# Optimization experiments

Hardware: AMD Instinct MI355X
Metric: run time of the kernel (lower is better)

The kernel has to match this reference:

```python
import jax, jax.numpy as jnp
import numpy as np

EPS = 1e-3  # kernel epsilon used in Performer generalized kernel
B, H, N, D, M = 1, 8, 1024, 64, 128  # batch, heads, seq, dim_heads, nb_features


def _gaussian_orthogonal_matrix(m, d, seed=0):
    # GaussianOrthogonalRandomMatrix with scaling=0: stacked QR blocks, rows
    # rescaled by chi-distributed norms of gaussian d-vectors.
    rng = np.random.default_rng(seed)
    blocks = []
    for _ in range(m // d):
        g = rng.standard_normal((d, d))
        qmat, _ = np.linalg.qr(g)
        blocks.append(qmat.T)
    proj = np.concatenate(blocks, axis=0)  # [m, d], orthonormal rows per block
    mult = np.linalg.norm(rng.standard_normal((m, d)), axis=1)  # chi norms
    return (mult[:, None] * proj).astype(np.float32)


def setup_inputs() -> dict:
    key = jax.random.key(0)
    kq, kk, kv = jax.random.split(key, 3)
    q = jax.random.normal(kq, (B, H, N, D), dtype=jnp.float32)
    k = jax.random.normal(kk, (B, H, N, D), dtype=jnp.float32)
    v = jax.random.normal(kv, (B, H, N, D), dtype=jnp.float32)
    proj = jnp.asarray(_gaussian_orthogonal_matrix(M, D))
    return {"q": q, "k": k, "v": v, "proj": proj}


def _generalized_kernel(x, proj):
    # kernel_fn(relu)( (x / d**0.25) @ proj^T ) + eps
    normalizer = 1.0 / (x.shape[-1] ** 0.25)
    xp = jnp.einsum('bhnd,md->bhnm', x * normalizer, proj)
    return jax.nn.relu(xp) + EPS


def reference(q, k, v, proj):
    qp = _generalized_kernel(q, proj)  # [B,H,N,M]
    kp = _generalized_kernel(k, proj)  # [B,H,N,M]
    # causal linear attention
    k_cumsum = jnp.cumsum(kp, axis=-2)                              # [B,H,N,M]
    context = jnp.einsum('bhnm,bhne->bhnme', kp, v)                 # [B,H,N,M,D]
    context = jnp.cumsum(context, axis=-3)                          # prefix sums over n
    context = context / k_cumsum[..., None]                         # normalize
    out = jnp.einsum('bhnme,bhnm->bhne', context, qp)               # [B,H,N,D]
    return out
```

## Files before the change

kernel.cpp:

```cpp
#include <hip/hip_runtime.h>

static constexpr int H = 8, N = 1024, D = 64, M = 128;
static constexpr float EPS = 1e-3f;
static constexpr float NORM = 0.35355339059327373f;

typedef __attribute__((ext_vector_type(8))) short short8;
typedef __attribute__((ext_vector_type(4))) float f32x4;

__device__ inline unsigned short f2bf(float x) {
    unsigned u = __float_as_uint(x);
    return (unsigned short)((u + 0x7fffu + ((u >> 16) & 1u)) >> 16);
}
__device__ inline float bf2f(unsigned short u) {
    return __uint_as_float(((unsigned)u) << 16);
}
__device__ inline ushort4 pack4(float4 g) {
    return (ushort4){f2bf(g.x), f2bf(g.y), f2bf(g.z), f2bf(g.w)};
}

__global__ __launch_bounds__(512) void k_projg(const float* __restrict__ q,
                                               const float* __restrict__ k,
                                               const float* __restrict__ proj,
                                               const float* __restrict__ v,
                                               unsigned short* __restrict__ qpb,
                                               unsigned short* __restrict__ kpb,
                                               unsigned short* __restrict__ Gpb,
                                               float* __restrict__ kpart) {
    __shared__ __align__(16) short smem[30208];
    short* projb = smem;
    short* xb = smem + 9216;
    short* obuf = smem + 13824;
    short* kpT = smem + 22528;
    short* vT = smem + 27648;
    const int tid = threadIdx.x;
    const int rblk = blockIdx.x;
    const int h = blockIdx.y;
    const int rowbase = h * N + rblk * 32;
    const int lane = tid & 63, wv = tid >> 6;
    const int rt = wv & 3, mh = wv >> 2;
    const int fr = lane & 15, fq = lane >> 4;

    {
        int r = tid >> 4, dq = tid & 15;
        float4 g = *(const float4*)&q[(rowbase + r) * D + dq * 4];
        float4 gk = *(const float4*)&k[(rowbase + r) * D + dq * 4];
        int rv = tid & 31, e4 = (tid >> 5) * 4;
        float4 gv = *(const float4*)&v[(rowbase + rv) * D + e4];
        g.x *= NORM; g.y *= NORM; g.z *= NORM; g.w *= NORM;
        *(ushort4*)&xb[r * 72 + dq * 4] = pack4(g);
        gk.x *= NORM; gk.y *= NORM; gk.z *= NORM; gk.w *= NORM;
        *(ushort4*)&xb[(32 + r) * 72 + dq * 4] = pack4(gk);
        vT[(e4 + 0) * 40 + rv] = (short)f2bf(gv.x);
        vT[(e4 + 1) * 40 + rv] = (short)f2bf(gv.y);
        vT[(e4 + 2) * 40 + rv] = (short)f2bf(gv.z);
        vT[(e4 + 3) * 40 + rv] = (short)f2bf(gv.w);
    }
    for (int i4 = tid; i4 < 2048; i4 += 512) {
        int m = i4 >> 4, dq = i4 & 15;
        *(ushort4*)&projb[m * 72 + dq * 4] = pack4(*(const float4*)&proj[i4 * 4]);
    }
    __syncthreads();

    f32x4 accp[4];
#pragma unroll
    for (int i = 0; i < 4; i++) accp[i] = (f32x4){0.f, 0.f, 0.f, 0.f};
#pragma unroll
    for (int kt = 0; kt < 2; kt++) {
        short8 a = *(const short8*)&xb[(16 * rt + fr) * 72 + kt * 32 + fq * 8];
#pragma unroll
        for (int i = 0; i < 4; i++) {
            const int mt = mh * 4 + i;
            short8 bb = *(const short8*)&projb[(16 * mt + fr) * 72 + kt * 32 + fq * 8];
            accp[i] = __builtin_amdgcn_mfma_f32_16x16x32_bf16(a, bb, accp[i], 0, 0, 0);
        }
    }
#pragma unroll
    for (int i = 0; i < 4; i++) {
        const int mt = mh * 4 + i;
#pragma unroll
        for (int reg = 0; reg < 4; reg++) {
            const int r = 16 * rt + fq * 4 + reg;
            const int m = 16 * mt + fr;
            unsigned short bv = f2bf(fmaxf(accp[i][reg], 0.f) + EPS);
            obuf[r * 136 + m] = (short)bv;
            if (rt >= 2) kpT[m * 40 + (r - 32)] = (short)bv;
        }
    }
    __syncthreads();

    for (int i = tid; i < 1024; i += 512) {
        int r = i >> 4, cu8 = i & 15;
        short8 val = *(const short8*)&obuf[r * 136 + cu8 * 8];
        unsigned short* g = (r < 32) ? &qpb[(rowbase + r) * M + cu8 * 8]
                                     : &kpb[(rowbase + r - 32) * M + cu8 * 8];
        *(short8*)g = val;
    }
    const int gb = h * 32 + rblk;
    {
        const int m = tid >> 2, qr = tid & 3;
        float part = 0.f;
#pragma unroll
        for (int r = 0; r < 8; r++)
            part += bf2f((unsigned short)kpT[m * 40 + qr * 8 + r]);
        float t2;
        t2 = __shfl_xor(part, 1, 4); part += t2;
        t2 = __shfl_xor(part, 2, 4); part += t2;
        if (qr == 0) kpart[gb * M + m] = part;
    }
    __syncthreads();

    f32x4 gacc[4];
#pragma unroll
    for (int et = 0; et < 4; et++) gacc[et] = (f32x4){0.f, 0.f, 0.f, 0.f};
    {
        short8 a = *(const short8*)&kpT[(16 * wv + fr) * 40 + fq * 8];
#pragma unroll
        for (int et = 0; et < 4; et++) {
            short8 bb = *(const short8*)&vT[(16 * et + fr) * 40 + fq * 8];
            gacc[et] = __builtin_amdgcn_mfma_f32_16x16x32_bf16(a, bb, gacc[et], 0, 0, 0);
        }
    }
#pragma unroll
    for (int et = 0; et < 4; et++)
#pragma unroll
        for (int reg = 0; reg < 4; reg++) {
            const int m = 16 * wv + fq * 4 + reg;
            obuf[m * 68 + 16 * et + fr] = (short)f2bf(gacc[et][reg]);
        }
    __syncthreads();
    for (int i = tid; i < 2048; i += 512) {
        int m = i >> 4, e4 = (i & 15) * 4;
        *(ushort4*)&Gpb[(gb * M + m) * D + e4] = *(const ushort4*)&obuf[m * 68 + e4];
    }
}

__global__ __launch_bounds__(512) void k_prefix(const float* __restrict__ kpart,
                                                const unsigned short* __restrict__ Gpb,
                                                float* __restrict__ zpre,
                                                unsigned short* __restrict__ S0pre) {
    const int tid = threadIdx.x;
    const int qr = tid & 3, s0 = qr * 8;
    const int eg = (blockIdx.x << 7) | (tid >> 2);
    const int h = eg >> 13, eb = eg & 8191;

    float g[8];
#pragma unroll
    for (int r = 0; r < 8; r++)
        g[r] = bf2f(Gpb[(h * 32 + s0 + r) * (M * D) + eb]);
    float part = 0.f;
#pragma unroll
    for (int r = 0; r < 8; r++) part += g[r];
    float incl = part, tt;
    tt = __shfl_up(incl, 1, 4); if (qr >= 1) incl += tt;
    tt = __shfl_up(incl, 2, 4); if (qr >= 2) incl += tt;
    tt = __shfl_up(incl, 1, 4);
    float a = (qr == 0) ? 0.f : tt;
    unsigned short o[8];
#pragma unroll
    for (int r = 0; r < 8; r++) {
        o[r] = f2bf(a);
        a += g[r];
    }
#pragma unroll
    for (int r = 0; r < 8; r++)
        S0pre[(h * 32 + s0 + r) * (M * D) + eb] = o[r];

    if (blockIdx.x < 8) {
        const int hh = blockIdx.x;
        const int m = tid >> 2;
        float kv[8];
#pragma unroll
        for (int r = 0; r < 8; r++) kv[r] = kpart[(hh * 32 + s0 + r) * M + m];
        float p2 = 0.f;
#pragma unroll
        for (int r = 0; r < 8; r++) p2 += kv[r];
        float i2 = p2, t2;
        t2 = __shfl_up(i2, 1, 4); if (qr >= 1) i2 += t2;
        t2 = __shfl_up(i2, 2, 4); if (qr >= 2) i2 += t2;
        t2 = __shfl_up(i2, 1, 4);
        float z = (qr == 0) ? 0.f : t2;
#pragma unroll
        for (int r = 0; r < 8; r++) {
            zpre[(hh * 32 + s0 + r) * M + m] = z;
            z += kv[r];
        }
    }
}

__global__ __launch_bounds__(512) void k_attn(const unsigned short* __restrict__ qpb,
                                              const unsigned short* __restrict__ kpb,
                                              const float* __restrict__ zpre,
                                              const unsigned short* __restrict__ S0pre,
                                              const float* __restrict__ v,
                                              float* __restrict__ out) {
    __shared__ __align__(16) short smem[25600];
    short* bufW = smem;
    short* bufK = smem + 4352;
    short* bufQ = smem + 8704;
    short* s0t  = smem + 13056;
    short* vT   = smem + 21760;
    short* bufP = smem + 24320;
    const int tid = threadIdx.x;
    const int b = blockIdx.x;
    const int h = b >> 5, s = b & 31;
    const int rowstart = h * N + s * 32;
    const int lane = tid & 63, wv = tid >> 6;
    const int rt = wv & 1, js = wv >> 1;
    const int fr = lane & 15, fq = lane >> 4;

    const int sj = tid >> 4, smu = tid & 15;
    short8 kpre = *(const short8*)&kpb[(rowstart + sj) * M + smu * 8];
    short8 qpre = *(const short8*)&qpb[(rowstart + sj) * M + smu * 8];
    const int pm = tid >> 2, peb = (tid & 3) * 16;
    const unsigned short* s0src = &S0pre[(h * 32 + s) * (M * D) + pm * D + peb];
    short8 s0a = *(const short8*)&s0src[0];
    short8 s0b = *(const short8*)&s0src[8];
    const int ve4 = (tid & 15) * 4;
    float4 gv = *(const float4*)&v[(rowstart + sj) * D + ve4];
    const float zinit = zpre[(h * 32 + s) * M + pm];

    *(short8*)&bufK[sj * 136 + smu * 8] = kpre;
    *(short8*)&bufQ[sj * 136 + smu * 8] = qpre;
#pragma unroll
    for (int j = 0; j < 8; j++) {
        s0t[(peb + j) * 136 + pm] = s0a[j];
        s0t[(peb + 8 + j) * 136 + pm] = s0b[j];
    }
    vT[(ve4 + 0) * 40 + sj] = (short)f2bf(gv.x);
    vT[(ve4 + 1) * 40 + sj] = (short)f2bf(gv.y);
    vT[(ve4 + 2) * 40 + sj] = (short)f2bf(gv.z);
    vT[(ve4 + 3) * 40 + sj] = (short)f2bf(gv.w);
    __syncthreads();

    {
        const int zm = tid >> 2, qr = tid & 3, r0 = qr * 8;
        float kv[8];
        float part = 0.f;
#pragma unroll
        for (int r = 0; r < 8; r++) {
            kv[r] = bf2f((unsigned short)bufK[(r0 + r) * 136 + zm]);
            part += kv[r];
        }
        float incl = part, t;
        t = __shfl_up(incl, 1, 4); if (qr >= 1) incl += t;
        t = __shfl_up(incl, 2, 4); if (qr >= 2) incl += t;
        t = __shfl_up(incl, 1, 4);
        float z = zinit + ((qr == 0) ? 0.f : t);
#pragma unroll
        for (int r = 0; r < 8; r++) {
            const int rr = r0 + r;
            z += kv[r];
            bufW[rr * 136 + zm] = (short)f2bf(
                bf2f((unsigned short)bufQ[rr * 136 + zm]) *
                __builtin_amdgcn_rcpf(z));
        }
    }
    __syncthreads();

    f32x4 acc2 = (f32x4){0.f, 0.f, 0.f, 0.f};
#pragma unroll
    for (int kt = 0; kt < 4; kt++) {
        short8 a = *(const short8*)&bufW[(16 * rt + fr) * 136 + kt * 32 + fq * 8];
        short8 bb = *(const short8*)&s0t[(16 * js + fr) * 136 + kt * 32 + fq * 8];
        acc2 = __builtin_amdgcn_mfma_f32_16x16x32_bf16(a, bb, acc2, 0, 0, 0);
    }
    if (wv < 4) {
        const int jt = wv >> 1;
        f32x4 acc1 = (f32x4){0.f, 0.f, 0.f, 0.f};
#pragma unroll
        for (int kt = 0; kt < 4; kt++) {
            short8 a = *(const short8*)&bufW[(16 * rt + fr) * 136 + kt * 32 + fq * 8];
            short8 bb = *(const short8*)&bufK[(16 * jt + fr) * 136 + kt * 32 + fq * 8];
            acc1 = __builtin_amdgcn_mfma_f32_16x16x32_bf16(a, bb, acc1, 0, 0, 0);
        }
        const int j = 16 * jt + fr;
#pragma unroll
        for (int reg = 0; reg < 4; reg++) {
            const int nloc = 16 * rt + fq * 4 + reg;
            float val = (j <= nloc) ? acc1[reg] : 0.f;
            bufP[nloc * 40 + j] = (short)f2bf(val);
        }
    }
    __syncthreads();

    {
        short8 a = *(const short8*)&bufP[(16 * rt + fr) * 40 + fq * 8];
        short8 bb = *(const short8*)&vT[(16 * js + fr) * 40 + fq * 8];
        acc2 = __builtin_amdgcn_mfma_f32_16x16x32_bf16(a, bb, acc2, 0, 0, 0);
    }

#pragma unroll
    for (int reg = 0; reg < 4; reg++) {
        out[(rowstart + 16 * rt + fq * 4 + reg) * D + 16 * js + fr] = acc2[reg];
    }
}

extern "C" void kernel_launch(void* const* d_in, const int* in_sizes, int n_in,
                              void* d_out, int out_size, void* d_ws, size_t ws_size,
                              hipStream_t stream) {
    const float* q = (const float*)d_in[0];
    const float* k = (const float*)d_in[1];
    const float* v = (const float*)d_in[2];
    const float* proj = (const float*)d_in[3];
    float* out = (float*)d_out;

    float* ws = (float*)d_ws;
    float* kpart = ws;
    unsigned short* qpb = (unsigned short*)(kpart + H * 32 * M);
    unsigned short* kpb = qpb + H * N * M;
    unsigned short* Gpb = kpb + H * N * M;
    float* zpre = (float*)(Gpb + H * 32 * M * D);
    unsigned short* S0pre = (unsigned short*)(zpre + H * 32 * M);

    k_projg<<<dim3(32, H), 512, 0, stream>>>(q, k, proj, v, qpb, kpb, Gpb,
                                             kpart);
    k_prefix<<<dim3(512), 512, 0, stream>>>(kpart, Gpb, zpre, S0pre);
    k_attn<<<dim3(H * 32), 512, 0, stream>>>(qpb, kpb, zpre, S0pre, v, out);
}
```

Baseline: 76.27 us.

## Split projection and attention kernels across feature/output halves with 256-thread blocks

The projection kernel now splits the 128 random features into two halves via a third grid dimension, and the attention kernel splits the 64 output columns into two halves via a second grid dimension. Each kernel uses 256-thread blocks with smaller shared memory, doubling the block count from 256 to 512 so more of the GPU's compute units are occupied. The cost is redundant work: each block in either kernel reloads its q/k rows, and each attention block recomputes the full causal score matrix and normalizer for its half.

```diff
diff --git a/kernel.cpp b/kernel.cpp
--- a/kernel.cpp
+++ b/kernel.cpp
@@ -18,7 +18,7 @@
     return (ushort4){f2bf(g.x), f2bf(g.y), f2bf(g.z), f2bf(g.w)};
 }
 
-__global__ __launch_bounds__(512) void k_projg(const float* __restrict__ q,
+__global__ __launch_bounds__(256) void k_projg(const float* __restrict__ q,
                                                const float* __restrict__ k,
                                                const float* __restrict__ proj,
                                                const float* __restrict__ v,
@@ -26,38 +26,48 @@
                                                unsigned short* __restrict__ kpb,
                                                unsigned short* __restrict__ Gpb,
                                                float* __restrict__ kpart) {
-    __shared__ __align__(16) short smem[30208];
+    __shared__ __align__(16) short smem[18944];
     short* projb = smem;
-    short* xb = smem + 9216;
-    short* obuf = smem + 13824;
-    short* kpT = smem + 22528;
-    short* vT = smem + 27648;
+    short* xb = smem + 4608;
+    short* obuf = smem + 9216;
+    short* kpT = smem + 13824;
+    short* vT = smem + 16384;
     const int tid = threadIdx.x;
     const int rblk = blockIdx.x;
     const int h = blockIdx.y;
+    const int mhf = blockIdx.z;
     const int rowbase = h * N + rblk * 32;
     const int lane = tid & 63, wv = tid >> 6;
-    const int rt = wv & 3, mh = wv >> 2;
+    const int rt = wv;
     const int fr = lane & 15, fq = lane >> 4;
 
     {
-        int r = tid >> 4, dq = tid & 15;
-        float4 g = *(const float4*)&q[(rowbase + r) * D + dq * 4];
-        float4 gk = *(const float4*)&k[(rowbase + r) * D + dq * 4];
-        int rv = tid & 31, e4 = (tid >> 5) * 4;
-        float4 gv = *(const float4*)&v[(rowbase + rv) * D + e4];
-        g.x *= NORM; g.y *= NORM; g.z *= NORM; g.w *= NORM;
-        *(ushort4*)&xb[r * 72 + dq * 4] = pack4(g);
-        gk.x *= NORM; gk.y *= NORM; gk.z *= NORM; gk.w *= NORM;
-        *(ushort4*)&xb[(32 + r) * 72 + dq * 4] = pack4(gk);
-        vT[(e4 + 0) * 40 + rv] = (short)f2bf(gv.x);
-        vT[(e4 + 1) * 40 + rv] = (short)f2bf(gv.y);
-        vT[(e4 + 2) * 40 + rv] = (short)f2bf(gv.z);
-        vT[(e4 + 3) * 40 + rv] = (short)f2bf(gv.w);
-    }
-    for (int i4 = tid; i4 < 2048; i4 += 512) {
-        int m = i4 >> 4, dq = i4 & 15;
-        *(ushort4*)&projb[m * 72 + dq * 4] = pack4(*(const float4*)&proj[i4 * 4]);
+        int r = tid >> 3, dq2 = (tid & 7) * 2;
+#pragma unroll
+        for (int t = 0; t < 2; t++) {
+            int dq = dq2 + t;
+            float4 g = *(const float4*)&q[(rowbase + r) * D + dq * 4];
+            float4 gk = *(const float4*)&k[(rowbase + r) * D + dq * 4];
+            g.x *= NORM; g.y *= NORM; g.z *= NORM; g.w *= NORM;
+            *(ushort4*)&xb[r * 72 + dq * 4] = pack4(g);
+            gk.x *= NORM; gk.y *= NORM; gk.z *= NORM; gk.w *= NORM;
+            *(ushort4*)&xb[(32 + r) * 72 + dq * 4] = pack4(gk);
+        }
+        int rv = tid & 31, e8 = (tid >> 5) * 8;
+#pragma unroll
+        for (int t = 0; t < 2; t++) {
+            int e4 = e8 + t * 4;
+            float4 gv = *(const float4*)&v[(rowbase + rv) * D + e4];
+            vT[(e4 + 0) * 40 + rv] = (short)f2bf(gv.x);
+            vT[(e4 + 1) * 40 + rv] = (short)f2bf(gv.y);
+            vT[(e4 + 2) * 40 + rv] = (short)f2bf(gv.z);
+            vT[(e4 + 3) * 40 + rv] = (short)f2bf(gv.w);
+        }
+    }
+    for (int i4 = tid; i4 < 1024; i4 += 256) {
+        int m_l = i4 >> 4, dq = i4 & 15;
+        *(ushort4*)&projb[m_l * 72 + dq * 4] =
+            pack4(*(const float4*)&proj[(mhf * 64 + m_l) * D + dq * 4]);
     }
     __syncthreads();
 
@@ -69,43 +79,42 @@
         short8 a = *(const short8*)&xb[(16 * rt + fr) * 72 + kt * 32 + fq * 8];
 #pragma unroll
         for (int i = 0; i < 4; i++) {
-            const int mt = mh * 4 + i;
-            short8 bb = *(const short8*)&projb[(16 * mt + fr) * 72 + kt * 32 + fq * 8];
+            short8 bb = *(const short8*)&projb[(16 * i + fr) * 72 + kt * 32 + fq * 8];
             accp[i] = __builtin_amdgcn_mfma_f32_16x16x32_bf16(a, bb, accp[i], 0, 0, 0);
         }
     }
 #pragma unroll
     for (int i = 0; i < 4; i++) {
-        const int mt = mh * 4 + i;
 #pragma unroll
         for (int reg = 0; reg < 4; reg++) {
             const int r = 16 * rt + fq * 4 + reg;
-            const int m = 16 * mt + fr;
+            const int m_l = 16 * i + fr;
             unsigned short bv = f2bf(fmaxf(accp[i][reg], 0.f) + EPS);
-            obuf[r * 136 + m] = (short)bv;
-            if (rt >= 2) kpT[m * 40 + (r - 32)] = (short)bv;
-        }
-    }
-    __syncthreads();
-
-    for (int i = tid; i < 1024; i += 512) {
-        int r = i >> 4, cu8 = i & 15;
-        short8 val = *(const short8*)&obuf[r * 136 + cu8 * 8];
-        unsigned short* g = (r < 32) ? &qpb[(rowbase + r) * M + cu8 * 8]
-                                     : &kpb[(rowbase + r - 32) * M + cu8 * 8];
+            obuf[r * 72 + m_l] = (short)bv;
+            if (rt >= 2) kpT[m_l * 40 + (r - 32)] = (short)bv;
+        }
+    }
+    __syncthreads();
+
+    for (int i = tid; i < 512; i += 256) {
+        int r = i >> 3, cu8 = i & 7;
+        short8 val = *(const short8*)&obuf[r * 72 + cu8 * 8];
+        unsigned short* g =
+            (r < 32) ? &qpb[(rowbase + r) * M + mhf * 64 + cu8 * 8]
+                     : &kpb[(rowbase + r - 32) * M + mhf * 64 + cu8 * 8];
         *(short8*)g = val;
     }
     const int gb = h * 32 + rblk;
     {
-        const int m = tid >> 2, qr = tid & 3;
+        const int m_l = tid >> 2, qr = tid & 3;
         float part = 0.f;
 #pragma unroll
         for (int r = 0; r < 8; r++)
-            part += bf2f((unsigned short)kpT[m * 40 + qr * 8 + r]);
+            part += bf2f((unsigned short)kpT[m_l * 40 + qr * 8 + r]);
         float t2;
         t2 = __shfl_xor(part, 1, 4); part += t2;
         t2 = __shfl_xor(part, 2, 4); part += t2;
-        if (qr == 0) kpart[gb * M + m] = part;
+        if (qr == 0) kpart[gb * M + mhf * 64 + m_l] = part;
     }
     __syncthreads();
 
@@ -124,13 +133,14 @@
     for (int et = 0; et < 4; et++)
 #pragma unroll
         for (int reg = 0; reg < 4; reg++) {
-            const int m = 16 * wv + fq * 4 + reg;
-            obuf[m * 68 + 16 * et + fr] = (short)f2bf(gacc[et][reg]);
-        }
-    __syncthreads();
-    for (int i = tid; i < 2048; i += 512) {
-        int m = i >> 4, e4 = (i & 15) * 4;
-        *(ushort4*)&Gpb[(gb * M + m) * D + e4] = *(const ushort4*)&obuf[m * 68 + e4];
+            const int m_l = 16 * wv + fq * 4 + reg;
+            obuf[m_l * 68 + 16 * et + fr] = (short)f2bf(gacc[et][reg]);
+        }
+    __syncthreads();
+    for (int i = tid; i < 1024; i += 256) {
+        int m_l = i >> 4, e4 = (i & 15) * 4;
+        *(ushort4*)&Gpb[(gb * M + mhf * 64 + m_l) * D + e4] =
+            *(const ushort4*)&obuf[m_l * 68 + e4];
     }
 }
 
@@ -187,67 +197,80 @@
     }
 }
 
-__global__ __launch_bounds__(512) void k_attn(const unsigned short* __restrict__ qpb,
+__global__ __launch_bounds__(256) void k_attn(const unsigned short* __restrict__ qpb,
                                               const unsigned short* __restrict__ kpb,
                                               const float* __restrict__ zpre,
                                               const unsigned short* __restrict__ S0pre,
                                               const float* __restrict__ v,
                                               float* __restrict__ out) {
-    __shared__ __align__(16) short smem[25600];
+    __shared__ __align__(16) short smem[19968];
     short* bufW = smem;
     short* bufK = smem + 4352;
     short* bufQ = smem + 8704;
     short* s0t  = smem + 13056;
-    short* vT   = smem + 21760;
-    short* bufP = smem + 24320;
+    short* vT   = smem + 17408;
+    short* bufP = smem + 18688;
     const int tid = threadIdx.x;
     const int b = blockIdx.x;
+    const int ehf = blockIdx.y;
     const int h = b >> 5, s = b & 31;
     const int rowstart = h * N + s * 32;
     const int lane = tid & 63, wv = tid >> 6;
     const int rt = wv & 1, js = wv >> 1;
     const int fr = lane & 15, fq = lane >> 4;
 
-    const int sj = tid >> 4, smu = tid & 15;
-    short8 kpre = *(const short8*)&kpb[(rowstart + sj) * M + smu * 8];
-    short8 qpre = *(const short8*)&qpb[(rowstart + sj) * M + smu * 8];
-    const int pm = tid >> 2, peb = (tid & 3) * 16;
-    const unsigned short* s0src = &S0pre[(h * 32 + s) * (M * D) + pm * D + peb];
+    short8 kpre[2], qpre[2];
+#pragma unroll
+    for (int t = 0; t < 2; t++) {
+        const int i = tid + t * 256;
+        const int sj = i >> 4, smu = i & 15;
+        kpre[t] = *(const short8*)&kpb[(rowstart + sj) * M + smu * 8];
+        qpre[t] = *(const short8*)&qpb[(rowstart + sj) * M + smu * 8];
+    }
+    const int pm = tid >> 1, pq = tid & 1;
+    const unsigned short* s0src =
+        &S0pre[(h * 32 + s) * (M * D) + pm * D + ehf * 32 + pq * 16];
     short8 s0a = *(const short8*)&s0src[0];
     short8 s0b = *(const short8*)&s0src[8];
-    const int ve4 = (tid & 15) * 4;
-    float4 gv = *(const float4*)&v[(rowstart + sj) * D + ve4];
-    const float zinit = zpre[(h * 32 + s) * M + pm];
-
-    *(short8*)&bufK[sj * 136 + smu * 8] = kpre;
-    *(short8*)&bufQ[sj * 136 + smu * 8] = qpre;
-#pragma unroll
-    for (int j = 0; j < 8; j++) {
-        s0t[(peb + j) * 136 + pm] = s0a[j];
-        s0t[(peb + 8 + j) * 136 + pm] = s0b[j];
-    }
-    vT[(ve4 + 0) * 40 + sj] = (short)f2bf(gv.x);
-    vT[(ve4 + 1) * 40 + sj] = (short)f2bf(gv.y);
-    vT[(ve4 + 2) * 40 + sj] = (short)f2bf(gv.z);
-    vT[(ve4 + 3) * 40 + sj] = (short)f2bf(gv.w);
-    __syncthreads();
-
-    {
-        const int zm = tid >> 2, qr = tid & 3, r0 = qr * 8;
-        float kv[8];
+    const int sj2 = tid >> 3, ve = (tid & 7) * 4;
+    float4 gv = *(const float4*)&v[(rowstart + sj2) * D + ehf * 32 + ve];
+    const int zm = tid >> 1, qh = tid & 1;
+    const float zinit = zpre[(h * 32 + s) * M + zm];
+
+#pragma unroll
+    for (int t = 0; t < 2; t++) {
+        const int i = tid + t * 256;
+        const int sj = i >> 4, smu = i & 15;
+        *(short8*)&bufK[sj * 136 + smu * 8] = kpre[t];
+        *(short8*)&bufQ[sj * 136 + smu * 8] = qpre[t];
+    }
+    {
+        const int el = pq * 16;
+#pragma unroll
+        for (int j = 0; j < 8; j++) {
+            s0t[(el + j) * 136 + pm] = s0a[j];
+            s0t[(el + 8 + j) * 136 + pm] = s0b[j];
+        }
+    }
+    vT[(ve + 0) * 40 + sj2] = (short)f2bf(gv.x);
+    vT[(ve + 1) * 40 + sj2] = (short)f2bf(gv.y);
+    vT[(ve + 2) * 40 + sj2] = (short)f2bf(gv.z);
+    vT[(ve + 3) * 40 + sj2] = (short)f2bf(gv.w);
+    __syncthreads();
+
+    {
+        const int r0 = qh * 16;
+        float kv[16];
         float part = 0.f;
 #pragma unroll
-        for (int r = 0; r < 8; r++) {
+        for (int r = 0; r < 16; r++) {
             kv[r] = bf2f((unsigned short)bufK[(r0 + r) * 136 + zm]);
             part += kv[r];
         }
-        float incl = part, t;
-        t = __shfl_up(incl, 1, 4); if (qr >= 1) incl += t;
-        t = __shfl_up(incl, 2, 4); if (qr >= 2) incl += t;
-        t = __shfl_up(incl, 1, 4);
-        float z = zinit + ((qr == 0) ? 0.f : t);
-#pragma unroll
-        for (int r = 0; r < 8; r++) {
+        float ex = __shfl_up(part, 1, 2);
+        float z = zinit + ((qh == 0) ? 0.f : ex);
+#pragma unroll
+        for (int r = 0; r < 16; r++) {
             const int rr = r0 + r;
             z += kv[r];
             bufW[rr * 136 + zm] = (short)f2bf(
@@ -264,8 +287,8 @@
         short8 bb = *(const short8*)&s0t[(16 * js + fr) * 136 + kt * 32 + fq * 8];
         acc2 = __builtin_amdgcn_mfma_f32_16x16x32_bf16(a, bb, acc2, 0, 0, 0);
     }
-    if (wv < 4) {
-        const int jt = wv >> 1;
+    {
+        const int jt = js;
         f32x4 acc1 = (f32x4){0.f, 0.f, 0.f, 0.f};
 #pragma unroll
         for (int kt = 0; kt < 4; kt++) {
@@ -291,7 +314,8 @@
 
 #pragma unroll
     for (int reg = 0; reg < 4; reg++) {
-        out[(rowstart + 16 * rt + fq * 4 + reg) * D + 16 * js + fr] = acc2[reg];
+        out[(rowstart + 16 * rt + fq * 4 + reg) * D + ehf * 32 + 16 * js + fr] =
+            acc2[reg];
     }
 }
 
@@ -312,8 +336,8 @@
     float* zpre = (float*)(Gpb + H * 32 * M * D);
     unsigned short* S0pre = (unsigned short*)(zpre + H * 32 * M);
 
-    k_projg<<<dim3(32, H), 512, 0, stream>>>(q, k, proj, v, qpb, kpb, Gpb,
-                                             kpart);
+    k_projg<<<dim3(32, H, 2), 256, 0, stream>>>(q, k, proj, v, qpb, kpb, Gpb,
+                                                kpart);
     k_prefix<<<dim3(512), 512, 0, stream>>>(kpart, Gpb, zpre, S0pre);
-    k_attn<<<dim3(H * 32), 512, 0, stream>>>(qpb, kpb, zpre, S0pre, v, out);
-}
+    k_attn<<<dim3(H * 32, 2), 256, 0, stream>>>(qpb, kpb, zpre, S0pre, v, out);
+}
```

After: 77.09 us. No clear change (+1.1%).
